# Performance work log

Measured on AMD Instinct MI355X. Metric: run time of the kernel, lower is better.

The kernel has to match this reference:

```python
import jax, jax.numpy as jnp
import numpy as np
from jax import lax

B, N, C = 8, 1024, 768
H = 12          # num_heads
D = C // H      # head_dim = 64
CH = 2          # c_h head-mix group size
G = H // CH     # number of head groups = 6
CQ = CK = 3     # conv kernel sizes


def setup_inputs() -> dict:
    key = jax.random.key(0)
    ks = jax.random.split(key, 13)
    s = 0.02
    return {
        "query": jax.random.normal(ks[0], (B, N, C), jnp.float32),
        "key": jax.random.normal(ks[1], (B, N, C), jnp.float32),
        "value": jax.random.normal(ks[2], (B, N, C), jnp.float32),
        "Wq": jax.random.normal(ks[3], (C, C), jnp.float32) * s,
        "bq": jax.random.normal(ks[4], (C,), jnp.float32) * s,
        "Wk": jax.random.normal(ks[5], (C, C), jnp.float32) * s,
        "bk": jax.random.normal(ks[6], (C,), jnp.float32) * s,
        "Wv": jax.random.normal(ks[7], (C, C), jnp.float32) * s,
        "bv": jax.random.normal(ks[8], (C,), jnp.float32) * s,
        "conv_w": jax.random.normal(ks[9], (H, 1, CQ, CK), jnp.float32) * 0.2,  # depthwise OIHW
        "head_mix": jax.random.normal(ks[10], (G, CH, CH), jnp.float32) * 0.5
                    + jnp.broadcast_to(jnp.eye(CH, dtype=jnp.float32), (G, CH, CH)),
        "Wo": jax.random.normal(ks[11], (C, C), jnp.float32) * s,
        "bo": jax.random.normal(ks[12], (C,), jnp.float32) * s,
    }


def reference(query, key, value, Wq, bq, Wk, bk, Wv, bv, conv_w, head_mix, Wo, bo):
    # projections (torch Linear: x @ W.T + b), then split heads -> (B, H, N, D)
    Q = (query @ Wq.T + bq).reshape(B, N, H, D).transpose(0, 2, 1, 3)
    K = (key   @ Wk.T + bk).reshape(B, N, H, D).transpose(0, 2, 1, 3)
    V = (value @ Wv.T + bv).reshape(B, N, H, D).transpose(0, 2, 1, 3)

    # scores: (B, H, Nq, Nk)
    scores = jnp.einsum('bhqd,bhkd->bhqk', Q, K) / jnp.sqrt(jnp.float32(D))

    # depthwise conv over the (Nq, Nk) score plane, groups = num_heads
    conv_attn = lax.conv_general_dilated(
        scores, conv_w,
        window_strides=(1, 1),
        padding=((CQ // 2, CQ // 2), (CK // 2, CK // 2)),
        dimension_numbers=('NCHW', 'OIHW', 'NCHW'),
        feature_group_count=H,
    )

    attn = jax.nn.softmax(conv_attn, axis=-1)  # (B, H, Nq, Nk)

    # cross-head mixing within groups of c_h heads
    attn_g = attn.reshape(B, G, CH, N, N)
    mixed = jnp.einsum('bghij,ghk->bgkij', attn_g, head_mix).reshape(B, H, N, N)

    out = jnp.einsum('bhqk,bhkd->bhqd', mixed, V)          # (B, H, N, D)
    out = out.transpose(0, 2, 1, 3).reshape(B, N, C)       # merge heads
    return out @ Wo.T + bo
```

## Files before the change

kernel.cpp:

```cpp
#include <hip/hip_runtime.h>
#include <stdint.h>

#define B_ 8
#define N_ 1024
#define C_ 768
#define H_ 12
#define G_ 6
#define QBLK 32
#define KSTEP 64
#define NQT 32
#define NKS 16

typedef __attribute__((ext_vector_type(8))) short bf16x8;
typedef __attribute__((ext_vector_type(8))) unsigned short u16x8;
typedef __attribute__((ext_vector_type(4))) float f32x4;

__device__ __forceinline__ float bf2f(unsigned short u) {
  return __uint_as_float(((unsigned)u) << 16);
}
__device__ __forceinline__ unsigned short f2bf(float f) {
  unsigned x = __float_as_uint(f);
  unsigned r = x + 0x7fffu + ((x >> 16) & 1u);
  return (unsigned short)(r >> 16);
}
__device__ __forceinline__ void gload16(const void* g, void* l) {
  __builtin_amdgcn_global_load_lds(
      (const __attribute__((address_space(1))) unsigned int*)g,
      (__attribute__((address_space(3))) unsigned int*)l, 16, 0, 0);
}

__global__ __launch_bounds__(256) void cvtX(
    const float* __restrict__ q, const float* __restrict__ k,
    const float* __restrict__ v, unsigned short* __restrict__ dst) {
  const float* src = (blockIdx.y == 0) ? q : (blockIdx.y == 1) ? k : v;
  unsigned short* d = dst + (size_t)blockIdx.y * ((size_t)B_ * N_ * C_);
  const size_t idx = ((size_t)blockIdx.x * 256 + threadIdx.x) * 8;
  const float4 f0 = *(const float4*)(src + idx);
  const float4 f1 = *(const float4*)(src + idx + 4);
  u16x8 o;
  o[0] = f2bf(f0.x); o[1] = f2bf(f0.y); o[2] = f2bf(f0.z); o[3] = f2bf(f0.w);
  o[4] = f2bf(f1.x); o[5] = f2bf(f1.y); o[6] = f2bf(f1.z); o[7] = f2bf(f1.w);
  *(u16x8*)(d + idx) = o;
}

__global__ __launch_bounds__(256) void cvtW(
    const float* __restrict__ wq, const float* __restrict__ wk,
    const float* __restrict__ wv, const float* __restrict__ wo,
    unsigned short* __restrict__ dst) {
  const float* src = (blockIdx.y == 0)   ? wq
                     : (blockIdx.y == 1) ? wk
                     : (blockIdx.y == 2) ? wv
                                         : wo;
  unsigned short* d = dst + (size_t)blockIdx.y * ((size_t)C_ * C_);
  const size_t idx = ((size_t)blockIdx.x * 256 + threadIdx.x) * 8;
  const float4 f0 = *(const float4*)(src + idx);
  const float4 f1 = *(const float4*)(src + idx + 4);
  u16x8 o;
  o[0] = f2bf(f0.x); o[1] = f2bf(f0.y); o[2] = f2bf(f0.z); o[3] = f2bf(f0.w);
  o[4] = f2bf(f1.x); o[5] = f2bf(f1.y); o[6] = f2bf(f1.z); o[7] = f2bf(f1.w);
  *(u16x8*)(d + idx) = o;
}

template <int MODE>
__device__ __forceinline__ void gemm_bf16(
    const unsigned short* __restrict__ X, const unsigned short* __restrict__ W,
    const float* __restrict__ bias, void* __restrict__ out, int row0, int col0,
    unsigned short* __restrict__ As, unsigned short* __restrict__ Bs) {
  const int tid = threadIdx.x;
  const int wid = tid >> 6, lane = tid & 63;
  const int lr = lane & 15, lk = (lane >> 4) << 3;
  const int qrow = (lane >> 4) << 2;
  const int wr = (wid & 1) << 6, wc = (wid >> 1) << 6;
  const int srow = (wid << 4) + (lane >> 2);
  const int scol = (lane & 3) << 3;
  const unsigned short* gA0 = X + (size_t)(row0 + srow) * C_ + scol;
  const unsigned short* gA1 = X + (size_t)(row0 + 64 + srow) * C_ + scol;
  const unsigned short* gB0 = W + (size_t)(col0 + srow) * C_ + scol;
  const unsigned short* gB1 = W + (size_t)(col0 + 64 + srow) * C_ + scol;
  unsigned short* lA0 = As + (wid << 9);
  unsigned short* lA1 = As + 2048 + (wid << 9);
  unsigned short* lB0 = Bs + (wid << 9);
  unsigned short* lB1 = Bs + 2048 + (wid << 9);
  f32x4 acc[4][4] = {};
  for (int k0 = 0; k0 < C_; k0 += 32) {
    gload16(gA0 + k0, lA0);
    gload16(gA1 + k0, lA1);
    gload16(gB0 + k0, lB0);
    gload16(gB1 + k0, lB1);
    __syncthreads();
    bf16x8 af[4], bg[4];
#pragma unroll
    for (int m = 0; m < 4; ++m)
      af[m] = *(const bf16x8*)&As[(wr + (m << 4) + lr) * 32 + lk];
#pragma unroll
    for (int n = 0; n < 4; ++n)
      bg[n] = *(const bf16x8*)&Bs[(wc + (n << 4) + lr) * 32 + lk];
#pragma unroll
    for (int m = 0; m < 4; ++m)
#pragma unroll
      for (int n = 0; n < 4; ++n)
        acc[m][n] = __builtin_amdgcn_mfma_f32_16x16x32_bf16(af[m], bg[n],
                                                            acc[m][n], 0, 0, 0);
    __syncthreads();
  }
#pragma unroll
  for (int m = 0; m < 4; ++m) {
#pragma unroll
    for (int n = 0; n < 4; ++n) {
      const int colc = col0 + wc + (n << 4) + lr;
      const float bv = bias[colc];
      if (MODE == 2) {
        const int r0 = row0 + wr + (m << 4) + qrow;
        const int bb = r0 >> 10, nn0 = r0 & 1023;
        const int hh = colc >> 6, dd = colc & 63;
        ushort4 pk;
        pk.x = f2bf(acc[m][n][0] + bv);
        pk.y = f2bf(acc[m][n][1] + bv);
        pk.z = f2bf(acc[m][n][2] + bv);
        pk.w = f2bf(acc[m][n][3] + bv);
        *(ushort4*)&((unsigned short*)out)[(((size_t)(bb * H_ + hh) << 6) + dd)
                                               * 1024 + nn0] = pk;
      } else {
#pragma unroll
        for (int q = 0; q < 4; ++q) {
          const int r = row0 + wr + (m << 4) + qrow + q;
          const float v = acc[m][n][q] + bv;
          if (MODE == 0) {
            ((float*)out)[(size_t)r * C_ + colc] = v;
          } else {
            const int bb = r >> 10, nn = r & 1023;
            const int hh = colc >> 6, dd = colc & 63;
            ((unsigned short*)out)[(((size_t)(bb * H_ + hh) << 10) + nn) * 64 +
                                   dd] = f2bf(v);
          }
        }
      }
    }
  }
}

__global__ __launch_bounds__(256) void proj3(
    const unsigned short* __restrict__ Xb, const unsigned short* __restrict__ Wb,
    const float* __restrict__ bq, const float* __restrict__ bk,
    const float* __restrict__ bv, unsigned short* Qb, unsigned short* Kb,
    unsigned short* Vt) {
  __shared__ __align__(16) unsigned short As[128 * 32];
  __shared__ __align__(16) unsigned short Bs[128 * 32];
  const int wg = blockIdx.x;
  const int nid = (wg & 7) * 144 + (wg >> 3);
  const int x = nid % 6, y = (nid / 6) & 63, z = nid / 384;
  const unsigned short* X = Xb + (size_t)z * B_ * N_ * C_;
  const unsigned short* W = Wb + (size_t)z * C_ * C_;
  if (z == 0)
    gemm_bf16<1>(X, W, bq, Qb, y << 7, x << 7, As, Bs);
  else if (z == 1)
    gemm_bf16<1>(X, W, bk, Kb, y << 7, x << 7, As, Bs);
  else
    gemm_bf16<2>(X, W, bv, Vt, y << 7, x << 7, As, Bs);
}

__global__ __launch_bounds__(256) void oproj(
    const unsigned short* __restrict__ X, const unsigned short* __restrict__ Wb,
    const float* __restrict__ bo, float* __restrict__ out) {
  __shared__ __align__(16) unsigned short As[128 * 32];
  __shared__ __align__(16) unsigned short Bs[128 * 32];
  const int wg = blockIdx.x;
  const int nid = (wg & 7) * 48 + (wg >> 3);
  const int x = nid % 6, y = nid / 6;
  gemm_bf16<0>(X, Wb + (size_t)3 * C_ * C_, bo, out, y << 7, x << 7, As, Bs);
}

__global__ __launch_bounds__(256, 3) void fused_attn(
    const unsigned short* __restrict__ Qb, const unsigned short* __restrict__ Kb,
    const unsigned short* __restrict__ Vt, const float* __restrict__ cw,
    const float* __restrict__ hm, unsigned short* __restrict__ pvout) {
  __shared__ __align__(16) unsigned char smem[43328];
  unsigned short* QPt = (unsigned short*)(smem + 33280);
  float* lsum = (float*)(smem + 43072);
#define KBASE(hh) (smem + (size_t)(hh)*8448)
#define VBASE(hh) (smem + 16896 + (size_t)(hh)*8192)

  const int wg = blockIdx.x;
  const int nid = (wg & 7) * 192 + (wg >> 3);
  const int qt = nid & 31;
  const int bg = nid >> 5;
  const int g = bg % G_, bb = bg / G_;
  const int i0 = qt << 5;

  const int tid = threadIdx.x;
  const int wid = tid >> 6, lane = tid & 63;
  const int lr = lane & 15, lg = lane >> 4;
  const int lk = lg << 3;

  const int h = wid >> 1, mt = wid & 1;

  const size_t HSTR = (size_t)N_ * 64;
  const unsigned short* Qz = Qb + (size_t)(bb * H_ + 2 * g) * HSTR;
  const unsigned short* Kz = Kb + (size_t)(bb * H_ + 2 * g) * HSTR;
  const unsigned short* Vz = Vt + (size_t)(bb * H_ + 2 * g) * HSTR;

  const int krow = tid >> 2, kd0 = (tid & 3) << 4;
  const int kc0 = (tid & 3) << 1;
  const int k2r = 64 + (tid >> 3), k2d = (tid & 7) << 3;
  const int vd = tid >> 2, vc0 = (tid & 3) << 4;

  u16x8 kreg[4], vreg[4];
  u16x8 kreg2[2];

  {
    const int gj = -1 + krow;
#pragma unroll
    for (int hh = 0; hh < 2; ++hh) {
      u16x8 a = {}, b = {};
      if (gj >= 0) {
        a = *(const u16x8*)(Kz + hh * HSTR + (size_t)gj * 64 + kd0);
        b = *(const u16x8*)(Kz + hh * HSTR + (size_t)gj * 64 + kd0 + 8);
      }
      kreg[2 * hh] = a; kreg[2 * hh + 1] = b;
    }
    if (tid < 16) {
      const int gj2 = -1 + k2r;
#pragma unroll
      for (int hh = 0; hh < 2; ++hh)
        kreg2[hh] = *(const u16x8*)(Kz + hh * HSTR + (size_t)gj2 * 64 + k2d);
    }
#pragma unroll
    for (int hh = 0; hh < 2; ++hh)
#pragma unroll
      for (int hf = 0; hf < 2; ++hf)
        vreg[2 * hh + hf] =
            *(const u16x8*)(Vz + hh * HSTR + (size_t)vd * 1024 + vc0 + (hf << 3));
  }

  {
    const int r = tid >> 3, d0 = (tid & 7) << 3;
    {
      const int gi = i0 - 1 + r;
#pragma unroll
      for (int hh = 0; hh < 2; ++hh) {
        u16x8 qv = {};
        if (gi >= 0 && gi < N_)
          qv = *(const u16x8*)(Qz + hh * HSTR + (size_t)gi * 64 + d0);
        *(u16x8*)&QPt[((size_t)(hh * 34 + r)) * 72 + d0] = qv;
      }
    }
    if (tid < 16) {
      const int r2 = 32 + (tid >> 3);
      const int gi = i0 - 1 + r2;
#pragma unroll
      for (int hh = 0; hh < 2; ++hh) {
        u16x8 qv = {};
        if (gi < N_) qv = *(const u16x8*)(Qz + hh * HSTR + (size_t)gi * 64 + d0);
        *(u16x8*)&QPt[((size_t)(hh * 34 + r2)) * 72 + d0] = qv;
      }
    }
  }
  __syncthreads();

  bf16x8 qtf[3][2];
  {
    float wc3[3][3];
#pragma unroll
    for (int a = 0; a < 3; ++a)
#pragma unroll
      for (int c = 0; c < 3; ++c)
        wc3[a][c] = cw[(2 * g + h) * 9 + a * 3 + c] *
                    (0.125f * 1.4426950408889634f);
    const int ribase = (mt << 4) + lr;
#pragma unroll
    for (int dh = 0; dh < 2; ++dh) {
      const u16x8 qa = *(const u16x8*)&QPt[((size_t)(h * 34 + ribase + 0)) * 72 +
                                           (dh << 5) + lk];
      const u16x8 qb = *(const u16x8*)&QPt[((size_t)(h * 34 + ribase + 1)) * 72 +
                                           (dh << 5) + lk];
      const u16x8 qc = *(const u16x8*)&QPt[((size_t)(h * 34 + ribase + 2)) * 72 +
                                           (dh << 5) + lk];
#pragma unroll
      for (int c = 0; c < 3; ++c) {
#pragma unroll
        for (int e = 0; e < 8; ++e) {
          const float v = bf2f(qa[e]) * wc3[0][c] + bf2f(qb[e]) * wc3[1][c] +
                          bf2f(qc[e]) * wc3[2][c];
          qtf[c][dh][e] = (short)f2bf(v);
        }
      }
    }
  }

  unsigned short* PtW = &QPt[(size_t)wid * 16 * 72];

  const unsigned char* kbB = KBASE(h) + lr * 128;
  int kofs[3][2];
#pragma unroll
  for (int c = 0; c < 3; ++c)
#pragma unroll
    for (int dh = 0; dh < 2; ++dh)
      kofs[c][dh] = (((((dh << 2) + lg) ^ ((lr + c) & 7)) << 4)) + c * 128;
  const unsigned char* vbB0 = VBASE(0) + lr * 128;
  const unsigned char* vbB1 = VBASE(1) + lr * 128;
  int vofs[2];
#pragma unroll
  for (int kj = 0; kj < 2; ++kj)
    vofs[kj] = ((((kj << 2) + lg) ^ (lr & 7)) << 4);

  float mreg = -3.0e38f, lreg = 0.f;
  f32x4 acc[2][4] = {};

  for (int s = 0; s < NKS; ++s) {
    {
      unsigned char* kr0 = KBASE(0) + krow * 128;
      unsigned char* kr1 = KBASE(1) + krow * 128;
      const int ksw = krow & 7;
      *(u16x8*)(kr0 + ((kc0 ^ ksw) << 4)) = kreg[0];
      *(u16x8*)(kr0 + (((kc0 + 1) ^ ksw) << 4)) = kreg[1];
      *(u16x8*)(kr1 + ((kc0 ^ ksw) << 4)) = kreg[2];
      *(u16x8*)(kr1 + (((kc0 + 1) ^ ksw) << 4)) = kreg[3];
      if (tid < 16) {
        const int k2sw = k2r & 7, k2c = tid & 7;
        *(u16x8*)(KBASE(0) + k2r * 128 + ((k2c ^ k2sw) << 4)) = kreg2[0];
        *(u16x8*)(KBASE(1) + k2r * 128 + ((k2c ^ k2sw) << 4)) = kreg2[1];
      }
      unsigned char* vr0 = VBASE(0) + vd * 128;
      unsigned char* vr1 = VBASE(1) + vd * 128;
      const int vsw = vd & 7, vcc = (tid & 3) << 1;
      *(u16x8*)(vr0 + ((vcc ^ vsw) << 4)) = vreg[0];
      *(u16x8*)(vr0 + (((vcc + 1) ^ vsw) << 4)) = vreg[1];
      *(u16x8*)(vr1 + ((vcc ^ vsw) << 4)) = vreg[2];
      *(u16x8*)(vr1 + (((vcc + 1) ^ vsw) << 4)) = vreg[3];
    }
    __syncthreads();

    if (s + 1 < NKS) {
      const int j1 = (s + 1) << 6;
      const int gj = j1 - 1 + krow;
#pragma unroll
      for (int hh = 0; hh < 2; ++hh) {
        kreg[2 * hh] = *(const u16x8*)(Kz + hh * HSTR + (size_t)gj * 64 + kd0);
        kreg[2 * hh + 1] =
            *(const u16x8*)(Kz + hh * HSTR + (size_t)gj * 64 + kd0 + 8);
      }
      if (tid < 16) {
        const int gj2 = j1 - 1 + k2r;
#pragma unroll
        for (int hh = 0; hh < 2; ++hh) {
          u16x8 a = {};
          if (gj2 < N_)
            a = *(const u16x8*)(Kz + hh * HSTR + (size_t)gj2 * 64 + k2d);
          kreg2[hh] = a;
        }
      }
#pragma unroll
      for (int hh = 0; hh < 2; ++hh)
#pragma unroll
        for (int hf = 0; hf < 2; ++hf)
          vreg[2 * hh + hf] = *(const u16x8*)(Vz + hh * HSTR + (size_t)vd * 1024 +
                                              j1 + vc0 + (hf << 3));
    }

    f32x4 racc[4] = {};
    __builtin_amdgcn_s_setprio(1);
#pragma unroll
    for (int c = 0; c < 3; ++c) {
#pragma unroll
      for (int dh = 0; dh < 2; ++dh) {
        const bf16x8 bq = qtf[c][dh];
#pragma unroll
        for (int nt = 0; nt < 4; ++nt) {
          const bf16x8 ak = *(const bf16x8*)(kbB + nt * 2048 + kofs[c][dh]);
          racc[nt] =
              __builtin_amdgcn_mfma_f32_16x16x32_bf16(ak, bq, racc[nt], 0, 0, 0);
        }
      }
    }
    __builtin_amdgcn_s_setprio(0);

    {
      float pmax = fmaxf(fmaxf(racc[0][0], racc[0][1]),
                         fmaxf(racc[0][2], racc[0][3]));
#pragma unroll
      for (int nt = 1; nt < 4; ++nt)
        pmax = fmaxf(pmax, fmaxf(fmaxf(racc[nt][0], racc[nt][1]),
                                 fmaxf(racc[nt][2], racc[nt][3])));
      pmax = fmaxf(pmax, __shfl_xor(pmax, 16));
      pmax = fmaxf(pmax, __shfl_xor(pmax, 32));
      if (__any(pmax > mreg + 8.f)) {
        const float mn = fmaxf(mreg, pmax);
        const float alpha = exp2f(mreg - mn);
        mreg = mn;
        lreg *= alpha;
        float a4[4];
#pragma unroll
        for (int q = 0; q < 4; ++q)
          a4[q] = __shfl(alpha, (lg << 4) | ((lg << 2) + q));
#pragma unroll
        for (int k2 = 0; k2 < 2; ++k2)
#pragma unroll
          for (int nt = 0; nt < 4; ++nt)
#pragma unroll
            for (int q = 0; q < 4; ++q) acc[k2][nt][q] *= a4[q];
      }
      float rs = 0.f;
#pragma unroll
      for (int nt = 0; nt < 4; ++nt)
#pragma unroll
        for (int q = 0; q < 4; ++q) {
          const float p = exp2f(racc[nt][q] - mreg);
          racc[nt][q] = p;
          rs += p;
        }
      rs += __shfl_xor(rs, 16);
      rs += __shfl_xor(rs, 32);
      lreg += rs;
#pragma unroll
      for (int nt = 0; nt < 4; ++nt) {
        ushort4 pw;
        pw.x = f2bf(racc[nt][0]); pw.y = f2bf(racc[nt][1]);
        pw.z = f2bf(racc[nt][2]); pw.w = f2bf(racc[nt][3]);
        *(ushort4*)&PtW[(size_t)lr * 72 + (nt << 4) + (lg << 2)] = pw;
      }
    }

    {
      bf16x8 paf[2];
      paf[0] = *(const bf16x8*)&PtW[(size_t)lr * 72 + lk];
      paf[1] = *(const bf16x8*)&PtW[(size_t)lr * 72 + 32 + lk];
      __builtin_amdgcn_s_setprio(1);
#pragma unroll
      for (int kj = 0; kj < 2; ++kj)
#pragma unroll
        for (int nt = 0; nt < 4; ++nt) {
          const bf16x8 bva = *(const bf16x8*)(vbB0 + nt * 2048 + vofs[kj]);
          const bf16x8 bvb = *(const bf16x8*)(vbB1 + nt * 2048 + vofs[kj]);
          acc[0][nt] = __builtin_amdgcn_mfma_f32_16x16x32_bf16(paf[kj], bva,
                                                               acc[0][nt], 0, 0, 0);
          acc[1][nt] = __builtin_amdgcn_mfma_f32_16x16x32_bf16(paf[kj], bvb,
                                                               acc[1][nt], 0, 0, 0);
        }
      __builtin_amdgcn_s_setprio(0);
    }
    __syncthreads();
  }

  if (lg == 0) lsum[h * 32 + (mt << 4) + lr] = lreg;
  __syncthreads();

  const float mw0 = hm[(g * 2 + h) * 2 + 0];
  const float mw1 = hm[(g * 2 + h) * 2 + 1];
  float* Os = (float*)smem;
  if (h == 1) {
#pragma unroll
    for (int q = 0; q < 4; ++q) {
      const int row = (mt << 4) + (lg << 2) + q;
      const float f0 = mw0 / lsum[32 + row];
      const float f1 = mw1 / lsum[32 + row];
#pragma unroll
      for (int nt = 0; nt < 4; ++nt) {
        Os[(size_t)(0 * 32 + row) * 68 + (nt << 4) + lr] = acc[0][nt][q] * f0;
        Os[(size_t)(1 * 32 + row) * 68 + (nt << 4) + lr] = acc[1][nt][q] * f1;
      }
    }
  }
  __syncthreads();
  if (h == 0) {
#pragma unroll
    for (int q = 0; q < 4; ++q) {
      const int row = (mt << 4) + (lg << 2) + q;
      const int gi = i0 + row;
      const float f0 = mw0 / lsum[row];
      const float f1 = mw1 / lsum[row];
#pragma unroll
      for (int nt = 0; nt < 4; ++nt) {
        const float v0 =
            acc[0][nt][q] * f0 + Os[(size_t)(0 * 32 + row) * 68 + (nt << 4) + lr];
        const float v1 =
            acc[1][nt][q] * f1 + Os[(size_t)(1 * 32 + row) * 68 + (nt << 4) + lr];
        pvout[(size_t)(bb * N_ + gi) * C_ + (2 * g + 0) * 64 + (nt << 4) + lr] =
            f2bf(v0);
        pvout[(size_t)(bb * N_ + gi) * C_ + (2 * g + 1) * 64 + (nt << 4) + lr] =
            f2bf(v1);
      }
    }
  }
#undef KBASE
#undef VBASE
}

extern "C" void kernel_launch(void* const* d_in, const int* in_sizes, int n_in,
                              void* d_out, int out_size, void* d_ws, size_t ws_size,
                              hipStream_t stream) {
  const float* query = (const float*)d_in[0];
  const float* key   = (const float*)d_in[1];
  const float* value = (const float*)d_in[2];
  const float* Wq = (const float*)d_in[3];
  const float* bq = (const float*)d_in[4];
  const float* Wk = (const float*)d_in[5];
  const float* bk = (const float*)d_in[6];
  const float* Wv = (const float*)d_in[7];
  const float* bv = (const float*)d_in[8];
  const float* cw = (const float*)d_in[9];
  const float* hm = (const float*)d_in[10];
  const float* Wo = (const float*)d_in[11];
  const float* bo = (const float*)d_in[12];
  float* out = (float*)d_out;

  char* ws = (char*)d_ws;
  const size_t SZ_BF = (size_t)B_ * H_ * N_ * 64 * 2;
  unsigned short* Qb = (unsigned short*)ws;
  unsigned short* Kb = (unsigned short*)(ws + SZ_BF);
  unsigned short* Vt = (unsigned short*)(ws + 2 * SZ_BF);
  unsigned short* pvb = (unsigned short*)(ws + 3 * SZ_BF);
  unsigned short* Xb = (unsigned short*)(ws + 4 * SZ_BF);
  unsigned short* Wb = (unsigned short*)(ws + 7 * SZ_BF);

  const dim3 blk(256);
  cvtX<<<dim3(3072, 3), blk, 0, stream>>>(query, key, value, Xb);
  cvtW<<<dim3(288, 4), blk, 0, stream>>>(Wq, Wk, Wv, Wo, Wb);
  proj3<<<dim3(1152), blk, 0, stream>>>(Xb, Wb, bq, bk, bv, Qb, Kb, Vt);
  fused_attn<<<dim3(1536), blk, 0, stream>>>(Qb, Kb, Vt, cw, hm, pvb);
  oproj<<<dim3(384), blk, 0, stream>>>(pvb, Wb, bo, out);
}
```

Before: 194.3 us.

## Double query tile per workgroup to reuse K/V tiles across two query subtiles

Each attention workgroup now handles 64 query rows instead of 32, with each wave processing two 16-row subtiles that share every K and V fragment loaded from LDS. This halves the number of K/V global-to-LDS transfers and LDS fragment reads per query row. In exchange the grid halves to 768 workgroups, register pressure roughly doubles for the accumulators (launch bounds lowered to 2 blocks per CU), and LDS use grows.

New measurement: 189.3 us. -2.6%, faster.

```diff
diff --git a/kernel.cpp b/kernel.cpp
--- a/kernel.cpp
+++ b/kernel.cpp
@@ -6,9 +6,9 @@
 #define C_ 768
 #define H_ 12
 #define G_ 6
-#define QBLK 32
+#define QBLK 64
 #define KSTEP 64
-#define NQT 32
+#define NQT 16
 #define NKS 16
 
 typedef __attribute__((ext_vector_type(8))) short bf16x8;
@@ -170,22 +170,22 @@
   gemm_bf16<0>(X, Wb + (size_t)3 * C_ * C_, bo, out, y << 7, x << 7, As, Bs);
 }
 
-__global__ __launch_bounds__(256, 3) void fused_attn(
+__global__ __launch_bounds__(256, 2) void fused_attn(
     const unsigned short* __restrict__ Qb, const unsigned short* __restrict__ Kb,
     const unsigned short* __restrict__ Vt, const float* __restrict__ cw,
     const float* __restrict__ hm, unsigned short* __restrict__ pvout) {
-  __shared__ __align__(16) unsigned char smem[43328];
+  __shared__ __align__(16) unsigned char smem[52800];
   unsigned short* QPt = (unsigned short*)(smem + 33280);
-  float* lsum = (float*)(smem + 43072);
+  float* lsum = (float*)(smem + 52288);
 #define KBASE(hh) (smem + (size_t)(hh)*8448)
 #define VBASE(hh) (smem + 16896 + (size_t)(hh)*8192)
 
   const int wg = blockIdx.x;
-  const int nid = (wg & 7) * 192 + (wg >> 3);
-  const int qt = nid & 31;
-  const int bg = nid >> 5;
+  const int nid = (wg & 7) * 96 + (wg >> 3);
+  const int qt = nid & 15;
+  const int bg = nid >> 4;
   const int g = bg % G_, bb = bg / G_;
-  const int i0 = qt << 5;
+  const int i0 = qt << 6;
 
   const int tid = threadIdx.x;
   const int wid = tid >> 6, lane = tid & 63;
@@ -233,31 +233,34 @@
   }
 
   {
-    const int r = tid >> 3, d0 = (tid & 7) << 3;
-    {
-      const int gi = i0 - 1 + r;
+    const int r = tid >> 2, d0 = (tid & 3) << 4;
+    const int gi = i0 - 1 + r;
+#pragma unroll
+    for (int hh = 0; hh < 2; ++hh) {
+      u16x8 qa = {}, qb = {};
+      if (gi >= 0 && gi < N_) {
+        qa = *(const u16x8*)(Qz + hh * HSTR + (size_t)gi * 64 + d0);
+        qb = *(const u16x8*)(Qz + hh * HSTR + (size_t)gi * 64 + d0 + 8);
+      }
+      *(u16x8*)&QPt[((size_t)(hh * 66 + r)) * 72 + d0] = qa;
+      *(u16x8*)&QPt[((size_t)(hh * 66 + r)) * 72 + d0 + 8] = qb;
+    }
+    if (tid < 16) {
+      const int r2 = 64 + (tid >> 3);
+      const int d0h = (tid & 7) << 3;
+      const int gi2 = i0 - 1 + r2;
 #pragma unroll
       for (int hh = 0; hh < 2; ++hh) {
         u16x8 qv = {};
-        if (gi >= 0 && gi < N_)
-          qv = *(const u16x8*)(Qz + hh * HSTR + (size_t)gi * 64 + d0);
-        *(u16x8*)&QPt[((size_t)(hh * 34 + r)) * 72 + d0] = qv;
-      }
-    }
-    if (tid < 16) {
-      const int r2 = 32 + (tid >> 3);
-      const int gi = i0 - 1 + r2;
-#pragma unroll
-      for (int hh = 0; hh < 2; ++hh) {
-        u16x8 qv = {};
-        if (gi < N_) qv = *(const u16x8*)(Qz + hh * HSTR + (size_t)gi * 64 + d0);
-        *(u16x8*)&QPt[((size_t)(hh * 34 + r2)) * 72 + d0] = qv;
+        if (gi2 < N_)
+          qv = *(const u16x8*)(Qz + hh * HSTR + (size_t)gi2 * 64 + d0h);
+        *(u16x8*)&QPt[((size_t)(hh * 66 + r2)) * 72 + d0h] = qv;
       }
     }
   }
   __syncthreads();
 
-  bf16x8 qtf[3][2];
+  bf16x8 qtf[2][3][2];
   {
     float wc3[3][3];
 #pragma unroll
@@ -266,28 +269,34 @@
       for (int c = 0; c < 3; ++c)
         wc3[a][c] = cw[(2 * g + h) * 9 + a * 3 + c] *
                     (0.125f * 1.4426950408889634f);
-    const int ribase = (mt << 4) + lr;
-#pragma unroll
-    for (int dh = 0; dh < 2; ++dh) {
-      const u16x8 qa = *(const u16x8*)&QPt[((size_t)(h * 34 + ribase + 0)) * 72 +
-                                           (dh << 5) + lk];
-      const u16x8 qb = *(const u16x8*)&QPt[((size_t)(h * 34 + ribase + 1)) * 72 +
-                                           (dh << 5) + lk];
-      const u16x8 qc = *(const u16x8*)&QPt[((size_t)(h * 34 + ribase + 2)) * 72 +
-                                           (dh << 5) + lk];
-#pragma unroll
-      for (int c = 0; c < 3; ++c) {
-#pragma unroll
-        for (int e = 0; e < 8; ++e) {
-          const float v = bf2f(qa[e]) * wc3[0][c] + bf2f(qb[e]) * wc3[1][c] +
-                          bf2f(qc[e]) * wc3[2][c];
-          qtf[c][dh][e] = (short)f2bf(v);
-        }
-      }
-    }
-  }
-
-  unsigned short* PtW = &QPt[(size_t)wid * 16 * 72];
+#pragma unroll
+    for (int qs = 0; qs < 2; ++qs) {
+      const int ribase = (mt << 5) + (qs << 4) + lr;
+#pragma unroll
+      for (int dh = 0; dh < 2; ++dh) {
+        const u16x8 qa =
+            *(const u16x8*)&QPt[((size_t)(h * 66 + ribase + 0)) * 72 +
+                                (dh << 5) + lk];
+        const u16x8 qb =
+            *(const u16x8*)&QPt[((size_t)(h * 66 + ribase + 1)) * 72 +
+                                (dh << 5) + lk];
+        const u16x8 qc =
+            *(const u16x8*)&QPt[((size_t)(h * 66 + ribase + 2)) * 72 +
+                                (dh << 5) + lk];
+#pragma unroll
+        for (int c = 0; c < 3; ++c) {
+#pragma unroll
+          for (int e = 0; e < 8; ++e) {
+            const float v = bf2f(qa[e]) * wc3[0][c] + bf2f(qb[e]) * wc3[1][c] +
+                            bf2f(qc[e]) * wc3[2][c];
+            qtf[qs][c][dh][e] = (short)f2bf(v);
+          }
+        }
+      }
+    }
+  }
+
+  unsigned short* PtW = &QPt[(size_t)wid * 2304];
 
   const unsigned char* kbB = KBASE(h) + lr * 128;
   int kofs[3][2];
@@ -303,8 +312,9 @@
   for (int kj = 0; kj < 2; ++kj)
     vofs[kj] = ((((kj << 2) + lg) ^ (lr & 7)) << 4);
 
-  float mreg = -3.0e38f, lreg = 0.f;
-  f32x4 acc[2][4] = {};
+  float mreg[2] = {-3.0e38f, -3.0e38f};
+  float lreg[2] = {0.f, 0.f};
+  f32x4 acc[2][2][4] = {};
 
   for (int s = 0; s < NKS; ++s) {
     {
@@ -357,73 +367,90 @@
                                               j1 + vc0 + (hf << 3));
     }
 
-    f32x4 racc[4] = {};
+    f32x4 racc[2][4] = {};
     __builtin_amdgcn_s_setprio(1);
 #pragma unroll
     for (int c = 0; c < 3; ++c) {
 #pragma unroll
       for (int dh = 0; dh < 2; ++dh) {
-        const bf16x8 bq = qtf[c][dh];
 #pragma unroll
         for (int nt = 0; nt < 4; ++nt) {
           const bf16x8 ak = *(const bf16x8*)(kbB + nt * 2048 + kofs[c][dh]);
-          racc[nt] =
-              __builtin_amdgcn_mfma_f32_16x16x32_bf16(ak, bq, racc[nt], 0, 0, 0);
+          racc[0][nt] = __builtin_amdgcn_mfma_f32_16x16x32_bf16(
+              ak, qtf[0][c][dh], racc[0][nt], 0, 0, 0);
+          racc[1][nt] = __builtin_amdgcn_mfma_f32_16x16x32_bf16(
+              ak, qtf[1][c][dh], racc[1][nt], 0, 0, 0);
         }
       }
     }
     __builtin_amdgcn_s_setprio(0);
 
     {
-      float pmax = fmaxf(fmaxf(racc[0][0], racc[0][1]),
-                         fmaxf(racc[0][2], racc[0][3]));
-#pragma unroll
-      for (int nt = 1; nt < 4; ++nt)
-        pmax = fmaxf(pmax, fmaxf(fmaxf(racc[nt][0], racc[nt][1]),
-                                 fmaxf(racc[nt][2], racc[nt][3])));
-      pmax = fmaxf(pmax, __shfl_xor(pmax, 16));
-      pmax = fmaxf(pmax, __shfl_xor(pmax, 32));
-      if (__any(pmax > mreg + 8.f)) {
-        const float mn = fmaxf(mreg, pmax);
-        const float alpha = exp2f(mreg - mn);
-        mreg = mn;
-        lreg *= alpha;
-        float a4[4];
-#pragma unroll
-        for (int q = 0; q < 4; ++q)
-          a4[q] = __shfl(alpha, (lg << 4) | ((lg << 2) + q));
-#pragma unroll
-        for (int k2 = 0; k2 < 2; ++k2)
-#pragma unroll
-          for (int nt = 0; nt < 4; ++nt)
-#pragma unroll
-            for (int q = 0; q < 4; ++q) acc[k2][nt][q] *= a4[q];
-      }
-      float rs = 0.f;
-#pragma unroll
-      for (int nt = 0; nt < 4; ++nt)
-#pragma unroll
-        for (int q = 0; q < 4; ++q) {
-          const float p = exp2f(racc[nt][q] - mreg);
-          racc[nt][q] = p;
-          rs += p;
-        }
-      rs += __shfl_xor(rs, 16);
-      rs += __shfl_xor(rs, 32);
-      lreg += rs;
-#pragma unroll
-      for (int nt = 0; nt < 4; ++nt) {
-        ushort4 pw;
-        pw.x = f2bf(racc[nt][0]); pw.y = f2bf(racc[nt][1]);
-        pw.z = f2bf(racc[nt][2]); pw.w = f2bf(racc[nt][3]);
-        *(ushort4*)&PtW[(size_t)lr * 72 + (nt << 4) + (lg << 2)] = pw;
+      float pmax[2];
+#pragma unroll
+      for (int qs = 0; qs < 2; ++qs) {
+        float pm = fmaxf(fmaxf(racc[qs][0][0], racc[qs][0][1]),
+                         fmaxf(racc[qs][0][2], racc[qs][0][3]));
+#pragma unroll
+        for (int nt = 1; nt < 4; ++nt)
+          pm = fmaxf(pm, fmaxf(fmaxf(racc[qs][nt][0], racc[qs][nt][1]),
+                               fmaxf(racc[qs][nt][2], racc[qs][nt][3])));
+        pm = fmaxf(pm, __shfl_xor(pm, 16));
+        pm = fmaxf(pm, __shfl_xor(pm, 32));
+        pmax[qs] = pm;
+      }
+      if (__any((pmax[0] > mreg[0] + 8.f) || (pmax[1] > mreg[1] + 8.f))) {
+#pragma unroll
+        for (int qs = 0; qs < 2; ++qs) {
+          const float mn = fmaxf(mreg[qs], pmax[qs]);
+          const float alpha = exp2f(mreg[qs] - mn);
+          mreg[qs] = mn;
+          lreg[qs] *= alpha;
+          float a4[4];
+#pragma unroll
+          for (int q = 0; q < 4; ++q)
+            a4[q] = __shfl(alpha, (lg << 4) | ((lg << 2) + q));
+#pragma unroll
+          for (int k2 = 0; k2 < 2; ++k2)
+#pragma unroll
+            for (int nt = 0; nt < 4; ++nt)
+#pragma unroll
+              for (int q = 0; q < 4; ++q) acc[k2][qs][nt][q] *= a4[q];
+        }
+      }
+#pragma unroll
+      for (int qs = 0; qs < 2; ++qs) {
+        float rs = 0.f;
+#pragma unroll
+        for (int nt = 0; nt < 4; ++nt)
+#pragma unroll
+          for (int q = 0; q < 4; ++q) {
+            const float p = exp2f(racc[qs][nt][q] - mreg[qs]);
+            racc[qs][nt][q] = p;
+            rs += p;
+          }
+        rs += __shfl_xor(rs, 16);
+        rs += __shfl_xor(rs, 32);
+        lreg[qs] += rs;
+#pragma unroll
+        for (int nt = 0; nt < 4; ++nt) {
+          ushort4 pw;
+          pw.x = f2bf(racc[qs][nt][0]); pw.y = f2bf(racc[qs][nt][1]);
+          pw.z = f2bf(racc[qs][nt][2]); pw.w = f2bf(racc[qs][nt][3]);
+          *(ushort4*)&PtW[(size_t)qs * 1152 + (size_t)lr * 72 + (nt << 4) +
+                          (lg << 2)] = pw;
+        }
       }
     }
 
     {
-      bf16x8 paf[2];
-      paf[0] = *(const bf16x8*)&PtW[(size_t)lr * 72 + lk];
-      paf[1] = *(const bf16x8*)&PtW[(size_t)lr * 72 + 32 + lk];
+      bf16x8 paf[2][2];
+#pragma unroll
+      for (int qs = 0; qs < 2; ++qs) {
+        paf[qs][0] = *(const bf16x8*)&PtW[(size_t)qs * 1152 + (size_t)lr * 72 + lk];
+        paf[qs][1] =
+            *(const bf16x8*)&PtW[(size_t)qs * 1152 + (size_t)lr * 72 + 32 + lk];
+      }
       __builtin_amdgcn_s_setprio(1);
 #pragma unroll
       for (int kj = 0; kj < 2; ++kj)
@@ -431,17 +458,23 @@
         for (int nt = 0; nt < 4; ++nt) {
           const bf16x8 bva = *(const bf16x8*)(vbB0 + nt * 2048 + vofs[kj]);
           const bf16x8 bvb = *(const bf16x8*)(vbB1 + nt * 2048 + vofs[kj]);
-          acc[0][nt] = __builtin_amdgcn_mfma_f32_16x16x32_bf16(paf[kj], bva,
-                                                               acc[0][nt], 0, 0, 0);
-          acc[1][nt] = __builtin_amdgcn_mfma_f32_16x16x32_bf16(paf[kj], bvb,
-                                                               acc[1][nt], 0, 0, 0);
+#pragma unroll
+          for (int qs = 0; qs < 2; ++qs) {
+            acc[0][qs][nt] = __builtin_amdgcn_mfma_f32_16x16x32_bf16(
+                paf[qs][kj], bva, acc[0][qs][nt], 0, 0, 0);
+            acc[1][qs][nt] = __builtin_amdgcn_mfma_f32_16x16x32_bf16(
+                paf[qs][kj], bvb, acc[1][qs][nt], 0, 0, 0);
+          }
         }
       __builtin_amdgcn_s_setprio(0);
     }
     __syncthreads();
   }
 
-  if (lg == 0) lsum[h * 32 + (mt << 4) + lr] = lreg;
+  if (lg == 0) {
+    lsum[h * 64 + (mt << 5) + lr] = lreg[0];
+    lsum[h * 64 + (mt << 5) + 16 + lr] = lreg[1];
+  }
   __syncthreads();
 
   const float mw0 = hm[(g * 2 + h) * 2 + 0];
@@ -449,37 +482,43 @@
   float* Os = (float*)smem;
   if (h == 1) {
 #pragma unroll
-    for (int q = 0; q < 4; ++q) {
-      const int row = (mt << 4) + (lg << 2) + q;
-      const float f0 = mw0 / lsum[32 + row];
-      const float f1 = mw1 / lsum[32 + row];
-#pragma unroll
-      for (int nt = 0; nt < 4; ++nt) {
-        Os[(size_t)(0 * 32 + row) * 68 + (nt << 4) + lr] = acc[0][nt][q] * f0;
-        Os[(size_t)(1 * 32 + row) * 68 + (nt << 4) + lr] = acc[1][nt][q] * f1;
-      }
-    }
+    for (int qs = 0; qs < 2; ++qs)
+#pragma unroll
+      for (int q = 0; q < 4; ++q) {
+        const int row = (mt << 5) + (qs << 4) + (lg << 2) + q;
+        const float f0 = mw0 / lsum[64 + row];
+        const float f1 = mw1 / lsum[64 + row];
+#pragma unroll
+        for (int nt = 0; nt < 4; ++nt) {
+          Os[(size_t)(0 * 64 + row) * 68 + (nt << 4) + lr] =
+              acc[0][qs][nt][q] * f0;
+          Os[(size_t)(1 * 64 + row) * 68 + (nt << 4) + lr] =
+              acc[1][qs][nt][q] * f1;
+        }
+      }
   }
   __syncthreads();
   if (h == 0) {
 #pragma unroll
-    for (int q = 0; q < 4; ++q) {
-      const int row = (mt << 4) + (lg << 2) + q;
-      const int gi = i0 + row;
-      const float f0 = mw0 / lsum[row];
-      const float f1 = mw1 / lsum[row];
-#pragma unroll
-      for (int nt = 0; nt < 4; ++nt) {
-        const float v0 =
-            acc[0][nt][q] * f0 + Os[(size_t)(0 * 32 + row) * 68 + (nt << 4) + lr];
-        const float v1 =
-            acc[1][nt][q] * f1 + Os[(size_t)(1 * 32 + row) * 68 + (nt << 4) + lr];
-        pvout[(size_t)(bb * N_ + gi) * C_ + (2 * g + 0) * 64 + (nt << 4) + lr] =
-            f2bf(v0);
-        pvout[(size_t)(bb * N_ + gi) * C_ + (2 * g + 1) * 64 + (nt << 4) + lr] =
-            f2bf(v1);
-      }
-    }
+    for (int qs = 0; qs < 2; ++qs)
+#pragma unroll
+      for (int q = 0; q < 4; ++q) {
+        const int row = (mt << 5) + (qs << 4) + (lg << 2) + q;
+        const int gi = i0 + row;
+        const float f0 = mw0 / lsum[row];
+        const float f1 = mw1 / lsum[row];
+#pragma unroll
+        for (int nt = 0; nt < 4; ++nt) {
+          const float v0 = acc[0][qs][nt][q] * f0 +
+                           Os[(size_t)(0 * 64 + row) * 68 + (nt << 4) + lr];
+          const float v1 = acc[1][qs][nt][q] * f1 +
+                           Os[(size_t)(1 * 64 + row) * 68 + (nt << 4) + lr];
+          pvout[(size_t)(bb * N_ + gi) * C_ + (2 * g + 0) * 64 + (nt << 4) +
+                lr] = f2bf(v0);
+          pvout[(size_t)(bb * N_ + gi) * C_ + (2 * g + 1) * 64 + (nt << 4) +
+                lr] = f2bf(v1);
+        }
+      }
   }
 #undef KBASE
 #undef VBASE
@@ -516,6 +555,6 @@
   cvtX<<<dim3(3072, 3), blk, 0, stream>>>(query, key, value, Xb);
   cvtW<<<dim3(288, 4), blk, 0, stream>>>(Wq, Wk, Wv, Wo, Wb);
   proj3<<<dim3(1152), blk, 0, stream>>>(Xb, Wb, bq, bk, bv, Qb, Kb, Vt);
-  fused_attn<<<dim3(1536), blk, 0, stream>>>(Qb, Kb, Vt, cw, hm, pvb);
+  fused_attn<<<dim3(768), blk, 0, stream>>>(Qb, Kb, Vt, cw, hm, pvb);
   oproj<<<dim3(384), blk, 0, stream>>>(pvb, Wb, bo, out);
 }
```

## Read V fragments directly from global memory and drop V/Q LDS staging

Applied to the files above, without the earlier changes.

The V tiles are no longer staged through shared memory. Each lane now loads its PV MFMA operands straight from global (transposed V) with a one-ahead software prefetch. Q rows are also read directly from global instead of via an LDS staging buffer and a barrier. Shared memory drops from about 43KB to 26KB, which could allow more resident workgroups, but the PV loop now waits on global/L2 latency inside the MFMA chain, and each 16-byte V load is strided by 2KB per row.

After: 298.2 us. +53.5%, slower.

```diff
diff --git a/kernel.cpp b/kernel.cpp
--- a/kernel.cpp
+++ b/kernel.cpp
@@ -174,11 +174,9 @@
     const unsigned short* __restrict__ Qb, const unsigned short* __restrict__ Kb,
     const unsigned short* __restrict__ Vt, const float* __restrict__ cw,
     const float* __restrict__ hm, unsigned short* __restrict__ pvout) {
-  __shared__ __align__(16) unsigned char smem[43328];
-  unsigned short* QPt = (unsigned short*)(smem + 33280);
-  float* lsum = (float*)(smem + 43072);
+  __shared__ __align__(16) unsigned char smem[26368];
+  float* lsum = (float*)(smem + 26112);
 #define KBASE(hh) (smem + (size_t)(hh)*8448)
-#define VBASE(hh) (smem + 16896 + (size_t)(hh)*8192)
 
   const int wg = blockIdx.x;
   const int nid = (wg & 7) * 192 + (wg >> 3);
@@ -202,9 +200,8 @@
   const int krow = tid >> 2, kd0 = (tid & 3) << 4;
   const int kc0 = (tid & 3) << 1;
   const int k2r = 64 + (tid >> 3), k2d = (tid & 7) << 3;
-  const int vd = tid >> 2, vc0 = (tid & 3) << 4;
-
-  u16x8 kreg[4], vreg[4];
+
+  u16x8 kreg[4];
   u16x8 kreg2[2];
 
   {
@@ -224,38 +221,7 @@
       for (int hh = 0; hh < 2; ++hh)
         kreg2[hh] = *(const u16x8*)(Kz + hh * HSTR + (size_t)gj2 * 64 + k2d);
     }
-#pragma unroll
-    for (int hh = 0; hh < 2; ++hh)
-#pragma unroll
-      for (int hf = 0; hf < 2; ++hf)
-        vreg[2 * hh + hf] =
-            *(const u16x8*)(Vz + hh * HSTR + (size_t)vd * 1024 + vc0 + (hf << 3));
-  }
-
-  {
-    const int r = tid >> 3, d0 = (tid & 7) << 3;
-    {
-      const int gi = i0 - 1 + r;
-#pragma unroll
-      for (int hh = 0; hh < 2; ++hh) {
-        u16x8 qv = {};
-        if (gi >= 0 && gi < N_)
-          qv = *(const u16x8*)(Qz + hh * HSTR + (size_t)gi * 64 + d0);
-        *(u16x8*)&QPt[((size_t)(hh * 34 + r)) * 72 + d0] = qv;
-      }
-    }
-    if (tid < 16) {
-      const int r2 = 32 + (tid >> 3);
-      const int gi = i0 - 1 + r2;
-#pragma unroll
-      for (int hh = 0; hh < 2; ++hh) {
-        u16x8 qv = {};
-        if (gi < N_) qv = *(const u16x8*)(Qz + hh * HSTR + (size_t)gi * 64 + d0);
-        *(u16x8*)&QPt[((size_t)(hh * 34 + r2)) * 72 + d0] = qv;
-      }
-    }
-  }
-  __syncthreads();
+  }
 
   bf16x8 qtf[3][2];
   {
@@ -267,27 +233,34 @@
         wc3[a][c] = cw[(2 * g + h) * 9 + a * 3 + c] *
                     (0.125f * 1.4426950408889634f);
     const int ribase = (mt << 4) + lr;
-#pragma unroll
-    for (int dh = 0; dh < 2; ++dh) {
-      const u16x8 qa = *(const u16x8*)&QPt[((size_t)(h * 34 + ribase + 0)) * 72 +
-                                           (dh << 5) + lk];
-      const u16x8 qb = *(const u16x8*)&QPt[((size_t)(h * 34 + ribase + 1)) * 72 +
-                                           (dh << 5) + lk];
-      const u16x8 qc = *(const u16x8*)&QPt[((size_t)(h * 34 + ribase + 2)) * 72 +
-                                           (dh << 5) + lk];
-#pragma unroll
-      for (int c = 0; c < 3; ++c) {
+    u16x8 qrows[3][2];
+#pragma unroll
+    for (int a = 0; a < 3; ++a) {
+      const int gi = i0 - 1 + ribase + a;
+      const bool ok = ((unsigned)gi < (unsigned)N_);
+#pragma unroll
+      for (int dh = 0; dh < 2; ++dh) {
+        u16x8 qv = {};
+        if (ok)
+          qv = *(const u16x8*)(Qz + h * HSTR + (size_t)gi * 64 + (dh << 5) + lk);
+        qrows[a][dh] = qv;
+      }
+    }
+#pragma unroll
+    for (int c = 0; c < 3; ++c)
+#pragma unroll
+      for (int dh = 0; dh < 2; ++dh)
 #pragma unroll
         for (int e = 0; e < 8; ++e) {
-          const float v = bf2f(qa[e]) * wc3[0][c] + bf2f(qb[e]) * wc3[1][c] +
-                          bf2f(qc[e]) * wc3[2][c];
+          const float v = bf2f(qrows[0][dh][e]) * wc3[0][c] +
+                          bf2f(qrows[1][dh][e]) * wc3[1][c] +
+                          bf2f(qrows[2][dh][e]) * wc3[2][c];
           qtf[c][dh][e] = (short)f2bf(v);
         }
-      }
-    }
-  }
-
-  unsigned short* PtW = &QPt[(size_t)wid * 16 * 72];
+  }
+
+  unsigned short* PtW =
+      (unsigned short*)(smem + 16896) + (size_t)wid * 1152;
 
   const unsigned char* kbB = KBASE(h) + lr * 128;
   int kofs[3][2];
@@ -296,17 +269,15 @@
 #pragma unroll
     for (int dh = 0; dh < 2; ++dh)
       kofs[c][dh] = (((((dh << 2) + lg) ^ ((lr + c) & 7)) << 4)) + c * 128;
-  const unsigned char* vbB0 = VBASE(0) + lr * 128;
-  const unsigned char* vbB1 = VBASE(1) + lr * 128;
-  int vofs[2];
-#pragma unroll
-  for (int kj = 0; kj < 2; ++kj)
-    vofs[kj] = ((((kj << 2) + lg) ^ (lr & 7)) << 4);
+
+  const unsigned short* vrow0 = Vz + (size_t)lr * 1024 + lk;
+  const unsigned short* vrow1 = vrow0 + HSTR;
 
   float mreg = -3.0e38f, lreg = 0.f;
   f32x4 acc[2][4] = {};
 
   for (int s = 0; s < NKS; ++s) {
+    const int j0 = s << 6;
     {
       unsigned char* kr0 = KBASE(0) + krow * 128;
       unsigned char* kr1 = KBASE(1) + krow * 128;
@@ -320,18 +291,11 @@
         *(u16x8*)(KBASE(0) + k2r * 128 + ((k2c ^ k2sw) << 4)) = kreg2[0];
         *(u16x8*)(KBASE(1) + k2r * 128 + ((k2c ^ k2sw) << 4)) = kreg2[1];
       }
-      unsigned char* vr0 = VBASE(0) + vd * 128;
-      unsigned char* vr1 = VBASE(1) + vd * 128;
-      const int vsw = vd & 7, vcc = (tid & 3) << 1;
-      *(u16x8*)(vr0 + ((vcc ^ vsw) << 4)) = vreg[0];
-      *(u16x8*)(vr0 + (((vcc + 1) ^ vsw) << 4)) = vreg[1];
-      *(u16x8*)(vr1 + ((vcc ^ vsw) << 4)) = vreg[2];
-      *(u16x8*)(vr1 + (((vcc + 1) ^ vsw) << 4)) = vreg[3];
     }
     __syncthreads();
 
     if (s + 1 < NKS) {
-      const int j1 = (s + 1) << 6;
+      const int j1 = j0 + KSTEP;
       const int gj = j1 - 1 + krow;
 #pragma unroll
       for (int hh = 0; hh < 2; ++hh) {
@@ -349,12 +313,6 @@
           kreg2[hh] = a;
         }
       }
-#pragma unroll
-      for (int hh = 0; hh < 2; ++hh)
-#pragma unroll
-        for (int hf = 0; hf < 2; ++hf)
-          vreg[2 * hh + hf] = *(const u16x8*)(Vz + hh * HSTR + (size_t)vd * 1024 +
-                                              j1 + vc0 + (hf << 3));
     }
 
     f32x4 racc[4] = {};
@@ -424,18 +382,26 @@
       bf16x8 paf[2];
       paf[0] = *(const bf16x8*)&PtW[(size_t)lr * 72 + lk];
       paf[1] = *(const bf16x8*)&PtW[(size_t)lr * 72 + 32 + lk];
+      const unsigned short* vp0 = vrow0 + j0;
+      const unsigned short* vp1 = vrow1 + j0;
+      bf16x8 pva = *(const bf16x8*)(vp0);
+      bf16x8 pvb = *(const bf16x8*)(vp1);
       __builtin_amdgcn_s_setprio(1);
 #pragma unroll
-      for (int kj = 0; kj < 2; ++kj)
-#pragma unroll
-        for (int nt = 0; nt < 4; ++nt) {
-          const bf16x8 bva = *(const bf16x8*)(vbB0 + nt * 2048 + vofs[kj]);
-          const bf16x8 bvb = *(const bf16x8*)(vbB1 + nt * 2048 + vofs[kj]);
-          acc[0][nt] = __builtin_amdgcn_mfma_f32_16x16x32_bf16(paf[kj], bva,
-                                                               acc[0][nt], 0, 0, 0);
-          acc[1][nt] = __builtin_amdgcn_mfma_f32_16x16x32_bf16(paf[kj], bvb,
-                                                               acc[1][nt], 0, 0, 0);
-        }
+      for (int t = 0; t < 8; ++t) {
+        const int kj = t >> 2, nt = t & 3;
+        const bf16x8 cva = pva, cvb = pvb;
+        if (t < 7) {
+          const int t1 = t + 1;
+          const size_t o = (size_t)(t1 & 3) * 16384 + ((t1 >> 2) << 5);
+          pva = *(const bf16x8*)(vp0 + o);
+          pvb = *(const bf16x8*)(vp1 + o);
+        }
+        acc[0][nt] = __builtin_amdgcn_mfma_f32_16x16x32_bf16(paf[kj], cva,
+                                                             acc[0][nt], 0, 0, 0);
+        acc[1][nt] = __builtin_amdgcn_mfma_f32_16x16x32_bf16(paf[kj], cvb,
+                                                             acc[1][nt], 0, 0, 0);
+      }
       __builtin_amdgcn_s_setprio(0);
     }
     __syncthreads();
@@ -482,7 +448,6 @@
     }
   }
 #undef KBASE
-#undef VBASE
 }
 
 extern "C" void kernel_launch(void* const* d_in, const int* in_sizes, int n_in,
```
